# Optimization experiments

Measured on AMD Instinct MI355X. Metric: run time of the kernel, lower is better.

The kernel has to match this reference:

```python
import jax, jax.numpy as jnp
import numpy as np

HIDDEN = 2048
TOKENS = 16384


def setup_inputs() -> dict:
    key = jax.random.key(0)
    kx, kw, kb, kg, kbe = jax.random.split(key, 5)
    x = jax.random.normal(kx, (TOKENS, HIDDEN), dtype=jnp.float32)
    # LayerNorm affine params
    ln_gamma = jnp.ones((HIDDEN,), dtype=jnp.float32)
    ln_beta = jnp.zeros((HIDDEN,), dtype=jnp.float32)
    # Linear params (PyTorch default init scale ~ U(-1/sqrt(d), 1/sqrt(d)))
    bound = 1.0 / np.sqrt(HIDDEN)
    W = jax.random.uniform(kw, (HIDDEN, HIDDEN), minval=-bound, maxval=bound, dtype=jnp.float32)
    b = jax.random.uniform(kb, (HIDDEN,), minval=-bound, maxval=bound, dtype=jnp.float32)
    return {"x": x, "ln_gamma": ln_gamma, "ln_beta": ln_beta, "W": W, "b": b}


def reference(x, ln_gamma, ln_beta, W, b):
    eps = 1e-5
    mu = jnp.mean(x, axis=-1, keepdims=True)
    var = jnp.mean(jnp.square(x - mu), axis=-1, keepdims=True)
    xn = (x - mu) * jax.lax.rsqrt(var + eps) * ln_gamma + ln_beta
    # Linear: y = xn @ W^T + b (W stored as [out, in] like torch)
    y = jnp.einsum('td,od->to', xn, W) + b
    # torch F.gelu default = exact erf gelu
    return jax.nn.gelu(y, approximate=False)
```

## Files before the change

kernel.cpp:

```cpp
#include <hip/hip_runtime.h>
#include <math.h>

#define TOKENS 16384
#define HIDDEN 2048
#define BM 256
#define BN 256
#define BK 64
#define NT (HIDDEN / BK)

typedef __attribute__((ext_vector_type(4))) float f32x4;
typedef __attribute__((ext_vector_type(8))) short s16x8;

__device__ __forceinline__ unsigned short f2bf(float f) {
  unsigned int u = __float_as_uint(f);
  u += 0x7fffu + ((u >> 16) & 1u);
  return (unsigned short)(u >> 16);
}

__device__ __forceinline__ float fast_gelu(float y) {
  float t = y * fmaf(y * y, 0.044715f, 1.0f);
  float e = __builtin_amdgcn_exp2f(-2.3022082f * t);
  return y * __builtin_amdgcn_rcpf(1.0f + e);
}

__global__ __launch_bounds__(256) void wconv_kernel(const float* __restrict__ W,
                                                    unsigned short* __restrict__ Wb) {
  const int n4 = (HIDDEN * HIDDEN) / 4;
  for (int i = blockIdx.x * 256 + threadIdx.x; i < n4; i += gridDim.x * 256) {
    float4 v = *(const float4*)(W + (size_t)i * 4);
    ushort4 o;
    o.x = f2bf(v.x); o.y = f2bf(v.y); o.z = f2bf(v.z); o.w = f2bf(v.w);
    *(ushort4*)(Wb + (size_t)i * 4) = o;
  }
}

__global__ __launch_bounds__(256) void ln_kernel(const float* __restrict__ x,
                                                 const float* __restrict__ gamma,
                                                 const float* __restrict__ beta,
                                                 unsigned short* __restrict__ xn) {
  const int row = blockIdx.x;
  const int t = threadIdx.x;
  const int wave = t >> 6, lane = t & 63;
  const float* xr = x + (size_t)row * HIDDEN + t * 8;
  float4 v0 = *(const float4*)(xr);
  float4 v1 = *(const float4*)(xr + 4);
  float xv[8] = {v0.x, v0.y, v0.z, v0.w, v1.x, v1.y, v1.z, v1.w};

  float s = 0.f, ss = 0.f;
#pragma unroll
  for (int j = 0; j < 8; ++j) { s += xv[j]; ss = fmaf(xv[j], xv[j], ss); }

#pragma unroll
  for (int off = 32; off > 0; off >>= 1) {
    s += __shfl_xor(s, off, 64);
    ss += __shfl_xor(ss, off, 64);
  }
  __shared__ float rs[4], rss[4];
  if (lane == 0) { rs[wave] = s; rss[wave] = ss; }
  __syncthreads();
  s = rs[0] + rs[1] + rs[2] + rs[3];
  ss = rss[0] + rss[1] + rss[2] + rss[3];

  const float mean = s * (1.0f / HIDDEN);
  const float var = ss * (1.0f / HIDDEN) - mean * mean;
  const float rstd = rsqrtf(var + 1e-5f);

  float4 g0 = *(const float4*)(gamma + t * 8);
  float4 g1 = *(const float4*)(gamma + t * 8 + 4);
  float4 b0 = *(const float4*)(beta + t * 8);
  float4 b1 = *(const float4*)(beta + t * 8 + 4);
  float gv[8] = {g0.x, g0.y, g0.z, g0.w, g1.x, g1.y, g1.z, g1.w};
  float bv[8] = {b0.x, b0.y, b0.z, b0.w, b1.x, b1.y, b1.z, b1.w};

  union { unsigned short h[8]; uint4 q; } pk;
#pragma unroll
  for (int j = 0; j < 8; ++j)
    pk.h[j] = f2bf((xv[j] - mean) * rstd * gv[j] + bv[j]);
  *(uint4*)(xn + (size_t)row * HIDDEN + t * 8) = pk.q;
}


#define GLOAD(gp, lp) __builtin_amdgcn_global_load_lds( \
    (const __attribute__((address_space(1))) unsigned int*)(gp), \
    (__attribute__((address_space(3))) unsigned int*)(lp), 16, 0, 0)

__global__ __launch_bounds__(512, 1) void gemm_kernel(const unsigned short* __restrict__ A,
                                                      const unsigned short* __restrict__ B,
                                                      const float* __restrict__ bias,
                                                      float* __restrict__ out) {
  __shared__ __attribute__((aligned(16))) char lds[131072];

  const int tid = threadIdx.x;
  const int lane = tid & 63;
  const int wave = tid >> 6;
  const int fr = lane & 15, hi = lane >> 4;

  const int wg = blockIdx.x;
  const int swz = (wg & 7) * 64 + (wg >> 3);
  const int tm = swz >> 3, tn = swz & 7;
  const int row0 = tm * BM, col0 = tn * BN;

  const int wmi = wave >> 2;
  const int wni = wave & 3;
  const int hB = wni >> 1, gB = wni & 1;

  const int rho = tid >> 3, sig = tid & 7;
  const int colgrp = ((sig ^ (rho & 7)) << 3);
  const unsigned short* Ap = A + (size_t)(row0 + rho) * HIDDEN + colgrp;
  const unsigned short* Bp = B + (size_t)(col0 + ((rho >> 5) << 6) + (rho & 31)) * HIDDEN + colgrp;
  const int ldsWaveOff = wave << 10;

  const int s0 = ((hi ^ (fr & 7)) << 4);
  const int s1 = (((4 + hi) ^ (fr & 7)) << 4);
  const int aRowB = fr << 7;
  const int bRowB = (((gB << 5) + fr) << 7);

  auto stageA = [&](int tt, int bufd, int qm) {
    const int tc = tt < NT ? tt : NT - 1;
    const unsigned short* g = Ap + (size_t)(qm << 6) * HIDDEN + tc * BK;
    GLOAD(g, lds + ((((bufd << 2) | qm) << 13)) + ldsWaveOff);
    GLOAD(g + (size_t)128 * HIDDEN, lds + ((((bufd << 2) | 2 | qm) << 13)) + ldsWaveOff);
  };
  auto stageB = [&](int tt, int bufd, int qn) {
    const int tc = tt < NT ? tt : NT - 1;
    const unsigned short* g = Bp + (size_t)(qn << 5) * HIDDEN + tc * BK;
    GLOAD(g, lds + 65536 + ((((bufd << 2) | qn) << 13)) + ldsWaveOff);
    GLOAD(g + (size_t)128 * HIDDEN, lds + 65536 + ((((bufd << 2) | 2 | qn) << 13)) + ldsWaveOff);
  };

  f32x4 acc[2][4][4] = {};
  s16x8 a[4][2], b[2][2];

  stageA(0, 0, 0); stageB(0, 0, 1); stageA(0, 0, 1); stageB(0, 0, 0);
  stageA(1, 1, 0); stageB(1, 1, 1);
  asm volatile("s_waitcnt vmcnt(4)" ::: "memory");
  __builtin_amdgcn_s_barrier();

  for (int t = 0; t < NT; ++t) {
    const int buf = t & 1;
    const char* Abase = lds + (((buf << 2) | (wmi << 1)) << 13);
    const char* Bbase = lds + 65536 + (((buf << 2) | (hB << 1)) << 13);

#pragma unroll
    for (int mi = 0; mi < 4; ++mi) {
      a[mi][0] = *(const s16x8*)(Abase + mi * 2048 + aRowB + s0);
      a[mi][1] = *(const s16x8*)(Abase + mi * 2048 + aRowB + s1);
    }
#pragma unroll
    for (int nj = 0; nj < 2; ++nj) {
      b[nj][0] = *(const s16x8*)(Bbase + nj * 2048 + bRowB + s0);
      b[nj][1] = *(const s16x8*)(Bbase + nj * 2048 + bRowB + s1);
    }
    stageA(t + 1, buf ^ 1, 1);
    asm volatile("s_waitcnt lgkmcnt(8)" ::: "memory");
    __builtin_amdgcn_s_barrier();
    asm volatile("s_waitcnt lgkmcnt(0)" ::: "memory");
    __builtin_amdgcn_s_setprio(1);
#pragma unroll
    for (int mi = 0; mi < 4; ++mi)
#pragma unroll
      for (int nj = 0; nj < 2; ++nj)
#pragma unroll
        for (int kk = 0; kk < 2; ++kk)
          acc[0][mi][nj] = __builtin_amdgcn_mfma_f32_16x16x32_bf16(a[mi][kk], b[nj][kk], acc[0][mi][nj], 0, 0, 0);
    __builtin_amdgcn_s_setprio(0);
    __builtin_amdgcn_s_barrier();

#pragma unroll
    for (int nj = 0; nj < 2; ++nj) {
      b[nj][0] = *(const s16x8*)(Bbase + 8192 + nj * 2048 + bRowB + s0);
      b[nj][1] = *(const s16x8*)(Bbase + 8192 + nj * 2048 + bRowB + s1);
    }
    stageB(t + 1, buf ^ 1, 0);
    __builtin_amdgcn_s_barrier();
    asm volatile("s_waitcnt lgkmcnt(0)" ::: "memory");
    __builtin_amdgcn_s_setprio(1);
#pragma unroll
    for (int mi = 0; mi < 4; ++mi)
#pragma unroll
      for (int nj = 0; nj < 2; ++nj)
#pragma unroll
        for (int kk = 0; kk < 2; ++kk)
          acc[0][mi][2 + nj] = __builtin_amdgcn_mfma_f32_16x16x32_bf16(a[mi][kk], b[nj][kk], acc[0][mi][2 + nj], 0, 0, 0);
    __builtin_amdgcn_s_setprio(0);
    __builtin_amdgcn_s_barrier();

#pragma unroll
    for (int mi = 0; mi < 4; ++mi) {
      a[mi][0] = *(const s16x8*)(Abase + 8192 + mi * 2048 + aRowB + s0);
      a[mi][1] = *(const s16x8*)(Abase + 8192 + mi * 2048 + aRowB + s1);
    }
    stageA(t + 2, buf, 0);
    asm volatile("s_waitcnt lgkmcnt(4)" ::: "memory");
    __builtin_amdgcn_s_barrier();
    asm volatile("s_waitcnt lgkmcnt(0)" ::: "memory");
    __builtin_amdgcn_s_setprio(1);
#pragma unroll
    for (int mi = 0; mi < 4; ++mi)
#pragma unroll
      for (int nj = 0; nj < 2; ++nj)
#pragma unroll
        for (int kk = 0; kk < 2; ++kk)
          acc[1][mi][2 + nj] = __builtin_amdgcn_mfma_f32_16x16x32_bf16(a[mi][kk], b[nj][kk], acc[1][mi][2 + nj], 0, 0, 0);
    __builtin_amdgcn_s_setprio(0);
    __builtin_amdgcn_s_barrier();

#pragma unroll
    for (int nj = 0; nj < 2; ++nj) {
      b[nj][0] = *(const s16x8*)(Bbase + nj * 2048 + bRowB + s0);
      b[nj][1] = *(const s16x8*)(Bbase + nj * 2048 + bRowB + s1);
    }
    stageB(t + 2, buf, 1);
    asm volatile("s_waitcnt vmcnt(4)" ::: "memory");
    __builtin_amdgcn_s_barrier();
    asm volatile("s_waitcnt lgkmcnt(0)" ::: "memory");
    __builtin_amdgcn_s_setprio(1);
#pragma unroll
    for (int mi = 0; mi < 4; ++mi)
#pragma unroll
      for (int nj = 0; nj < 2; ++nj)
#pragma unroll
        for (int kk = 0; kk < 2; ++kk)
          acc[1][mi][nj] = __builtin_amdgcn_mfma_f32_16x16x32_bf16(a[mi][kk], b[nj][kk], acc[1][mi][nj], 0, 0, 0);
    __builtin_amdgcn_s_setprio(0);
    __builtin_amdgcn_s_barrier();
  }

  asm volatile("s_waitcnt vmcnt(0)" ::: "memory");

  float bcol[4];
#pragma unroll
  for (int ni = 0; ni < 4; ++ni)
    bcol[ni] = bias[col0 + (wni << 6) + ni * 16 + fr];

#pragma unroll
  for (int qm = 0; qm < 2; ++qm)
#pragma unroll
    for (int mi = 0; mi < 4; ++mi)
#pragma unroll
      for (int ni = 0; ni < 4; ++ni) {
        const int c = col0 + (wni << 6) + ni * 16 + fr;
#pragma unroll
        for (int j = 0; j < 4; ++j) {
          const int r = row0 + wmi * 128 + qm * 64 + mi * 16 + hi * 4 + j;
          float y = acc[qm][mi][ni][j] + bcol[ni];
          out[(size_t)r * HIDDEN + c] = fast_gelu(y);
        }
      }
}

extern "C" void kernel_launch(void* const* d_in, const int* in_sizes, int n_in,
                              void* d_out, int out_size, void* d_ws, size_t ws_size,
                              hipStream_t stream) {
  const float* x     = (const float*)d_in[0];
  const float* gamma = (const float*)d_in[1];
  const float* beta  = (const float*)d_in[2];
  const float* W     = (const float*)d_in[3];
  const float* bias  = (const float*)d_in[4];
  float* out = (float*)d_out;

  unsigned short* xn = (unsigned short*)d_ws;
  unsigned short* wb = (unsigned short*)((char*)d_ws + (size_t)TOKENS * HIDDEN * 2);

  hipLaunchKernelGGL(wconv_kernel, dim3(1024), dim3(256), 0, stream, W, wb);
  hipLaunchKernelGGL(ln_kernel, dim3(TOKENS), dim3(256), 0, stream, x, gamma, beta, xn);
  hipLaunchKernelGGL(gemm_kernel, dim3((TOKENS / BM) * (HIDDEN / BN)), dim3(512), 0, stream,
                     xn, wb, bias, out);
}
```

Before: 176.2 us.

## Fuse LayerNorm into GEMM prologue, removing separate LN kernel launch

Drops the standalone LayerNorm kernel. Each GEMM workgroup now normalizes its own 256 rows of x to bf16 at the start, writes them to the xn workspace, waits on a barrier, then runs the original GEMM reading xn. This removes one kernel launch and its scheduling gap. The cost is that the 8 column-tile workgroups sharing a row tile each redo the same LayerNorm, so x is read and xn written up to 8 times. That work runs serially before the matmul pipeline starts, and the blocks race benignly on identical xn values.

```diff
diff --git a/kernel.cpp b/kernel.cpp
--- a/kernel.cpp
+++ b/kernel.cpp
@@ -34,59 +34,17 @@
   }
 }
 
-__global__ __launch_bounds__(256) void ln_kernel(const float* __restrict__ x,
-                                                 const float* __restrict__ gamma,
-                                                 const float* __restrict__ beta,
-                                                 unsigned short* __restrict__ xn) {
-  const int row = blockIdx.x;
-  const int t = threadIdx.x;
-  const int wave = t >> 6, lane = t & 63;
-  const float* xr = x + (size_t)row * HIDDEN + t * 8;
-  float4 v0 = *(const float4*)(xr);
-  float4 v1 = *(const float4*)(xr + 4);
-  float xv[8] = {v0.x, v0.y, v0.z, v0.w, v1.x, v1.y, v1.z, v1.w};
-
-  float s = 0.f, ss = 0.f;
-#pragma unroll
-  for (int j = 0; j < 8; ++j) { s += xv[j]; ss = fmaf(xv[j], xv[j], ss); }
-
-#pragma unroll
-  for (int off = 32; off > 0; off >>= 1) {
-    s += __shfl_xor(s, off, 64);
-    ss += __shfl_xor(ss, off, 64);
-  }
-  __shared__ float rs[4], rss[4];
-  if (lane == 0) { rs[wave] = s; rss[wave] = ss; }
-  __syncthreads();
-  s = rs[0] + rs[1] + rs[2] + rs[3];
-  ss = rss[0] + rss[1] + rss[2] + rss[3];
-
-  const float mean = s * (1.0f / HIDDEN);
-  const float var = ss * (1.0f / HIDDEN) - mean * mean;
-  const float rstd = rsqrtf(var + 1e-5f);
-
-  float4 g0 = *(const float4*)(gamma + t * 8);
-  float4 g1 = *(const float4*)(gamma + t * 8 + 4);
-  float4 b0 = *(const float4*)(beta + t * 8);
-  float4 b1 = *(const float4*)(beta + t * 8 + 4);
-  float gv[8] = {g0.x, g0.y, g0.z, g0.w, g1.x, g1.y, g1.z, g1.w};
-  float bv[8] = {b0.x, b0.y, b0.z, b0.w, b1.x, b1.y, b1.z, b1.w};
-
-  union { unsigned short h[8]; uint4 q; } pk;
-#pragma unroll
-  for (int j = 0; j < 8; ++j)
-    pk.h[j] = f2bf((xv[j] - mean) * rstd * gv[j] + bv[j]);
-  *(uint4*)(xn + (size_t)row * HIDDEN + t * 8) = pk.q;
-}
-
 
 #define GLOAD(gp, lp) __builtin_amdgcn_global_load_lds( \
     (const __attribute__((address_space(1))) unsigned int*)(gp), \
     (__attribute__((address_space(3))) unsigned int*)(lp), 16, 0, 0)
 
-__global__ __launch_bounds__(512, 1) void gemm_kernel(const unsigned short* __restrict__ A,
+__global__ __launch_bounds__(512, 1) void gemm_kernel(const float* __restrict__ x,
+                                                      const float* __restrict__ gamma,
+                                                      const float* __restrict__ beta,
                                                       const unsigned short* __restrict__ B,
                                                       const float* __restrict__ bias,
+                                                      unsigned short* __restrict__ xn,
                                                       float* __restrict__ out) {
   __shared__ __attribute__((aligned(16))) char lds[131072];
 
@@ -104,9 +62,55 @@
   const int wni = wave & 3;
   const int hB = wni >> 1, gB = wni & 1;
 
+  {
+    const float rh = 1.0f / HIDDEN;
+    for (int rr = 0; rr < 32; ++rr) {
+      const int r = row0 + (wave << 5) + rr;
+      const float* xr = x + (size_t)r * HIDDEN;
+      float xv[32];
+      float s = 0.f, ss = 0.f;
+#pragma unroll
+      for (int k = 0; k < 4; ++k) {
+        const float4 v0 = *(const float4*)(xr + lane * 8 + k * 512);
+        const float4 v1 = *(const float4*)(xr + lane * 8 + k * 512 + 4);
+        xv[k*8+0]=v0.x; xv[k*8+1]=v0.y; xv[k*8+2]=v0.z; xv[k*8+3]=v0.w;
+        xv[k*8+4]=v1.x; xv[k*8+5]=v1.y; xv[k*8+6]=v1.z; xv[k*8+7]=v1.w;
+      }
+#pragma unroll
+      for (int j = 0; j < 32; ++j) { s += xv[j]; ss = fmaf(xv[j], xv[j], ss); }
+#pragma unroll
+      for (int off = 32; off > 0; off >>= 1) {
+        s += __shfl_xor(s, off, 64);
+        ss += __shfl_xor(ss, off, 64);
+      }
+      const float mean = s * rh;
+      const float rstd = rsqrtf(ss * rh - mean * mean + 1e-5f);
+      unsigned short* xw = xn + (size_t)r * HIDDEN;
+#pragma unroll
+      for (int k = 0; k < 4; ++k) {
+        const float4 g0 = *(const float4*)(gamma + lane * 8 + k * 512);
+        const float4 g1 = *(const float4*)(gamma + lane * 8 + k * 512 + 4);
+        const float4 e0 = *(const float4*)(beta + lane * 8 + k * 512);
+        const float4 e1 = *(const float4*)(beta + lane * 8 + k * 512 + 4);
+        union { unsigned short h[8]; uint4 q; } pk;
+        pk.h[0] = f2bf((xv[k*8+0]-mean)*rstd*g0.x + e0.x);
+        pk.h[1] = f2bf((xv[k*8+1]-mean)*rstd*g0.y + e0.y);
+        pk.h[2] = f2bf((xv[k*8+2]-mean)*rstd*g0.z + e0.z);
+        pk.h[3] = f2bf((xv[k*8+3]-mean)*rstd*g0.w + e0.w);
+        pk.h[4] = f2bf((xv[k*8+4]-mean)*rstd*g1.x + e1.x);
+        pk.h[5] = f2bf((xv[k*8+5]-mean)*rstd*g1.y + e1.y);
+        pk.h[6] = f2bf((xv[k*8+6]-mean)*rstd*g1.z + e1.z);
+        pk.h[7] = f2bf((xv[k*8+7]-mean)*rstd*g1.w + e1.w);
+        *(uint4*)(xw + lane * 8 + k * 512) = pk.q;
+      }
+    }
+    asm volatile("s_waitcnt vmcnt(0)" ::: "memory");
+    __builtin_amdgcn_s_barrier();
+  }
+
   const int rho = tid >> 3, sig = tid & 7;
   const int colgrp = ((sig ^ (rho & 7)) << 3);
-  const unsigned short* Ap = A + (size_t)(row0 + rho) * HIDDEN + colgrp;
+  const unsigned short* Ap = xn + (size_t)(row0 + rho) * HIDDEN + colgrp;
   const unsigned short* Bp = B + (size_t)(col0 + ((rho >> 5) << 6) + (rho & 31)) * HIDDEN + colgrp;
   const int ldsWaveOff = wave << 10;
 
@@ -263,7 +267,6 @@
   unsigned short* wb = (unsigned short*)((char*)d_ws + (size_t)TOKENS * HIDDEN * 2);
 
   hipLaunchKernelGGL(wconv_kernel, dim3(1024), dim3(256), 0, stream, W, wb);
-  hipLaunchKernelGGL(ln_kernel, dim3(TOKENS), dim3(256), 0, stream, x, gamma, beta, xn);
   hipLaunchKernelGGL(gemm_kernel, dim3((TOKENS / BM) * (HIDDEN / BN)), dim3(512), 0, stream,
-                     xn, wb, bias, out);
-}
+                     x, gamma, beta, wb, bias, xn, out);
+}
```

Result: slower. 243.4 us (+38.1%).
